# Kernel optimization log

Hardware: AMD Instinct MI355X
Metric: run time of the kernel (lower is better)

The kernel has to match this reference:

```python
import jax, jax.numpy as jnp
import numpy as np

B, S, D, F, E, TOP_K = 4, 1024, 512, 2048, 16, 2
TEMPERATURE = 0.5
STD = 0.02


def setup_inputs() -> dict:
    key = jax.random.key(0)
    ks = jax.random.split(key, 9)
    f32 = jnp.float32
    return {
        "x": jax.random.normal(ks[0], (B, S, D), f32),
        # router gate: Linear(D, D//2) -> ReLU -> Linear(D//2, E)
        "gate_w1": jax.random.normal(ks[1], (D, D // 2), f32) * STD,
        "gate_b1": jnp.zeros((D // 2,), f32),
        "gate_w2": jax.random.normal(ks[2], (D // 2, E), f32) * STD,
        "gate_b2": jnp.zeros((E,), f32),
        # stacked expert weights (E experts, each D->F->D)
        "up_w": jax.random.normal(ks[3], (E, D, F), f32) * STD,
        "up_b": jnp.zeros((E, F), f32),
        "down_w": jax.random.normal(ks[4], (E, F, D), f32) * STD,
        "down_b": jnp.zeros((E, D), f32),
    }


def reference(x, gate_w1, gate_b1, gate_w2, gate_b2, up_w, up_b, down_w, down_b):
    num_experts = up_w.shape[0]
    # ---- router ----
    h = jax.nn.relu(x @ gate_w1 + gate_b1)                      # [B,S,D//2]
    scores = h @ gate_w2 + gate_b2                              # [B,S,E]
    routing_probs = jax.nn.softmax(scores / TEMPERATURE, axis=-1)
    # load-balance loss: MSE(mean usage, uniform)
    batch_usage = routing_probs.mean(axis=(0, 1))               # [E]
    load_balance_loss = jnp.mean((batch_usage - 1.0 / num_experts) ** 2)
    # ---- top-k routing weights, renormalized via softmax over selected scores ----
    top_vals, top_idx = jax.lax.top_k(routing_probs, TOP_K)     # [B,S,K]
    top_probs = jax.nn.softmax(top_vals, axis=-1)               # [B,S,K]
    # scatter per-token top-k probs into dense [B,S,E] combine weights
    expert_probs = jnp.einsum(
        "bske,bsk->bse", jax.nn.one_hot(top_idx, num_experts, dtype=x.dtype), top_probs
    )
    # ---- every expert computed densely on all tokens, masked combine (faithful to source) ----
    hid = jax.nn.gelu(
        jnp.einsum("bsd,edf->ebsf", x, up_w) + up_b[:, None, None, :],
        approximate=False,
    )                                                            # [E,B,S,F]
    expert_out = jnp.einsum("ebsf,efd->ebsd", hid, down_w) + down_b[:, None, None, :]
    output = jnp.einsum("ebsd,bse->bsd", expert_out, expert_probs)  # [B,S,D]
    return output, load_balance_loss, routing_probs
```

## Files before the change

kernel.cpp:

```cpp
#include <hip/hip_runtime.h>
#include <hip/hip_bf16.h>

#define NTOK 4096
#define DIM  512
#define DH   256
#define NE   16
#define FF   2048
#define CAP  8192
#define MAXTILES 80
#define TEMP_INV 2.0f

#define OUT_LOSS  (NTOK * DIM)
#define OUT_PROBS (NTOK * DIM + 1)

#define WS_CNT    0
#define WS_USAGE  64
#define WS_NTILES 128
#define WS_DESC   256
#define WS_WTS    1024
#define WS_LISTS  36864
#define WS_H      (1ull<<20)
#define WS_G      (1ull<<20)
#define WS_TUP    (16ull<<20)
#define WS_PAIR   (16ull<<20)
#define WS_TDN    (48ull<<20)
#define WS_HID    (80ull<<20)

typedef __attribute__((ext_vector_type(8))) short bf16x8;
typedef __attribute__((ext_vector_type(8))) unsigned short u16x8;
typedef __attribute__((ext_vector_type(4))) float f32x4;

__device__ __forceinline__ unsigned short f2bf(float f) {
  union { float f; unsigned u; } c; c.f = f;
  return (unsigned short)((c.u + 0x7FFFu + ((c.u >> 16) & 1u)) >> 16);
}

#define GLOAD16(gp, lp) __builtin_amdgcn_global_load_lds( \
    (const __attribute__((address_space(1))) void*)(gp), \
    (__attribute__((address_space(3))) void*)(lp), 16, 0, 0)

__launch_bounds__(64)
__global__ void prep_kernel(const float* __restrict__ x,
                            const float* __restrict__ w1,
                            const float* __restrict__ b1,
                            const float* __restrict__ up_w,
                            const float* __restrict__ down_w,
                            float* __restrict__ H,
                            unsigned short* __restrict__ Tup,
                            unsigned short* __restrict__ Tdn) {
  __shared__ __align__(16) float As[32 * 72];
  __shared__ __align__(16) float Bs[32 * 40];
  int bx = blockIdx.x, tid = threadIdx.x;

  if (bx < 512) {
    int tok0 = (bx >> 3) * 64, n0 = (bx & 7) * 32;
    int ty = tid >> 3, tx = tid & 7;
    float acc[8][4];
#pragma unroll
    for (int r = 0; r < 8; ++r)
#pragma unroll
      for (int c = 0; c < 4; ++c) acc[r][c] = 0.f;

    for (int kc = 0; kc < 16; ++kc) {
      int k0 = kc * 32;
      {
        const float* xp = x + (size_t)(tok0 + tid) * DIM + k0;
#pragma unroll
        for (int q = 0; q < 8; ++q) {
          float4 v = *(const float4*)(xp + q * 4);
          As[(q * 4 + 0) * 72 + tid] = v.x;
          As[(q * 4 + 1) * 72 + tid] = v.y;
          As[(q * 4 + 2) * 72 + tid] = v.z;
          As[(q * 4 + 3) * 72 + tid] = v.w;
        }
      }
      {
        int kk = tid >> 1, ns = (tid & 1) * 16;
#pragma unroll
        for (int j = 0; j < 4; ++j)
          *(float4*)&Bs[kk * 40 + ns + j * 4] =
              *(const float4*)(w1 + (size_t)(k0 + kk) * DH + n0 + ns + j * 4);
      }
      __syncthreads();
#pragma unroll 8
      for (int k = 0; k < 32; ++k) {
        float4 a0 = *(const float4*)&As[k * 72 + ty * 8];
        float4 a1 = *(const float4*)&As[k * 72 + ty * 8 + 4];
        float4 b  = *(const float4*)&Bs[k * 40 + tx * 4];
#pragma unroll
        for (int c = 0; c < 4; ++c) {
          float bv = (c == 0) ? b.x : (c == 1) ? b.y : (c == 2) ? b.z : b.w;
          acc[0][c] = fmaf(a0.x, bv, acc[0][c]);
          acc[1][c] = fmaf(a0.y, bv, acc[1][c]);
          acc[2][c] = fmaf(a0.z, bv, acc[2][c]);
          acc[3][c] = fmaf(a0.w, bv, acc[3][c]);
          acc[4][c] = fmaf(a1.x, bv, acc[4][c]);
          acc[5][c] = fmaf(a1.y, bv, acc[5][c]);
          acc[6][c] = fmaf(a1.z, bv, acc[6][c]);
          acc[7][c] = fmaf(a1.w, bv, acc[7][c]);
        }
      }
      __syncthreads();
    }
    float4 bb = *(const float4*)(b1 + n0 + tx * 4);
#pragma unroll
    for (int r = 0; r < 8; ++r) {
      float4 o;
      o.x = fmaxf(acc[r][0] + bb.x, 0.f);
      o.y = fmaxf(acc[r][1] + bb.y, 0.f);
      o.z = fmaxf(acc[r][2] + bb.z, 0.f);
      o.w = fmaxf(acc[r][3] + bb.w, 0.f);
      *(float4*)(H + (size_t)(tok0 + ty * 8 + r) * DH + n0 + tx * 4) = o;
    }
  } else {
    int cb = bx - 512;
    const float* src; unsigned short* dst; int stride;
    if (cb < 4096) {
      int e = cb >> 8, kc = (cb >> 5) & 7, nb = cb & 31;
      src = up_w + (size_t)e * DIM * FF + (size_t)kc * 64 * FF + nb * 64;
      dst = Tup + ((size_t)(e * 8 + kc) * FF + nb * 64) * 64;
      stride = FF;
    } else {
      cb -= 4096;
      int e = cb >> 8, kc = (cb >> 3) & 31, nb = cb & 7;
      src = down_w + (size_t)e * FF * DIM + (size_t)kc * 64 * DIM + nb * 64;
      dst = Tdn + ((size_t)(e * 32 + kc) * DIM + nb * 64) * 64;
      stride = DIM;
    }
    const float* s = src + tid;
    unsigned short* drow = dst + (size_t)tid * 64;
    int sx = tid & 7;
#pragma unroll
    for (int g = 0; g < 8; ++g) {
      u16x8 pk;
#pragma unroll
      for (int j = 0; j < 8; ++j) pk[j] = f2bf(s[(size_t)(g * 8 + j) * stride]);
      *(u16x8*)(drow + ((g ^ sx) << 3)) = pk;
    }
  }
}

__launch_bounds__(256)
__global__ void score_kernel(const float* __restrict__ H,
                             const float* __restrict__ w2,
                             const float* __restrict__ b2,
                             float* __restrict__ out,
                             int* __restrict__ cnt,
                             float* __restrict__ usage,
                             float* __restrict__ wts,
                             int* __restrict__ lists) {
  __shared__ __align__(16) float hs[16][260];
  __shared__ __align__(16) float w2t[16][260];
  __shared__ float ps[16][NE];
  __shared__ float us[4][NE];
  int tid = threadIdx.x;
  int tok0 = blockIdx.x * 16;
  {
    int r = tid >> 4, seg = tid & 15;
    const float* hp = H + (size_t)(tok0 + r) * DH + seg * 16;
    *(float4*)&hs[r][seg * 16 + 0]  = *(const float4*)(hp + 0);
    *(float4*)&hs[r][seg * 16 + 4]  = *(const float4*)(hp + 4);
    *(float4*)&hs[r][seg * 16 + 8]  = *(const float4*)(hp + 8);
    *(float4*)&hs[r][seg * 16 + 12] = *(const float4*)(hp + 12);
  }
  {
    float4 a = *(const float4*)(w2 + (size_t)tid * 16 + 0);
    float4 b = *(const float4*)(w2 + (size_t)tid * 16 + 4);
    float4 c = *(const float4*)(w2 + (size_t)tid * 16 + 8);
    float4 d = *(const float4*)(w2 + (size_t)tid * 16 + 12);
    w2t[0][tid] = a.x;  w2t[1][tid] = a.y;  w2t[2][tid] = a.z;  w2t[3][tid] = a.w;
    w2t[4][tid] = b.x;  w2t[5][tid] = b.y;  w2t[6][tid] = b.z;  w2t[7][tid] = b.w;
    w2t[8][tid] = c.x;  w2t[9][tid] = c.y;  w2t[10][tid] = c.z; w2t[11][tid] = c.w;
    w2t[12][tid] = d.x; w2t[13][tid] = d.y; w2t[14][tid] = d.z; w2t[15][tid] = d.w;
  }
  __syncthreads();
  int t = tid >> 4, e = tid & 15;
  float s = b2[e];
#pragma unroll 4
  for (int j4 = 0; j4 < 64; ++j4) {
    float4 hv = *(const float4*)&hs[t][j4 * 4];
    float4 wv = *(const float4*)&w2t[e][j4 * 4];
    s = fmaf(hv.x, wv.x, fmaf(hv.y, wv.y, fmaf(hv.z, wv.z, fmaf(hv.w, wv.w, s))));
  }
  s *= TEMP_INV;
  float m = s;
#pragma unroll
  for (int d = 1; d < 16; d <<= 1) m = fmaxf(m, __shfl_xor(m, d));
  float p = expf(s - m);
  float sum = p;
#pragma unroll
  for (int d = 1; d < 16; d <<= 1) sum += __shfl_xor(sum, d);
  float prob = p / sum;
  out[OUT_PROBS + (size_t)(tok0 + t) * NE + e] = prob;
  ps[t][e] = prob;
  float v = prob;
  v += __shfl_xor(v, 16);
  v += __shfl_xor(v, 32);
  if ((tid & 63) < 16) us[tid >> 6][e] = v;
  __syncthreads();
  if (tid < 16) atomicAdd(&usage[tid], us[0][tid] + us[1][tid] + us[2][tid] + us[3][tid]);

  if (tid < 16) {
    int tt = tid;
    float v1 = -1.f; int i1 = 0;
    for (int ee = 0; ee < NE; ++ee) { float pv = ps[tt][ee]; if (pv > v1) { v1 = pv; i1 = ee; } }
    float v2 = -1.f; int i2 = 0;
    for (int ee = 0; ee < NE; ++ee) { if (ee == i1) continue; float pv = ps[tt][ee]; if (pv > v2) { v2 = pv; i2 = ee; } }
    float mm = fmaxf(v1, v2);
    float e0 = expf(v1 - mm), e1 = expf(v2 - mm);
    float rs = 1.f / (e0 + e1);
    int gt = tok0 + tt;
    wts[2 * gt]     = e0 * rs;
    wts[2 * gt + 1] = e1 * rs;
    int p1 = atomicAdd(&cnt[i1], 1);
    lists[i1 * CAP + p1] = 2 * gt;
    int p2 = atomicAdd(&cnt[i2], 1);
    lists[i2 * CAP + p2] = 2 * gt + 1;
  }
}

__global__ void sched_kernel(const int* __restrict__ cnt,
                             const float* __restrict__ usage,
                             int* __restrict__ ntiles,
                             int2* __restrict__ desc,
                             float* __restrict__ out_loss) {
  int lane = threadIdx.x;
  int e = lane & 15;
  int c = (lane < 16) ? cnt[e] : 0;
  int tl = (c + 127) >> 7;
  int v = tl;
#pragma unroll
  for (int d = 1; d < 16; d <<= 1) {
    int u = __shfl_up(v, d);
    if (lane >= d) v += u;
  }
  int excl = v - tl;
  int tot = __shfl(v, 15);
  if (lane == 0) *ntiles = tot;
  if (lane < 16) {
    for (int i = 0; i < tl; ++i) desc[excl + i] = make_int2(e, i << 7);
    float d0 = usage[e] * (1.f / 4096.f) - (1.f / 16.f);
    float ls = d0 * d0;
#pragma unroll
    for (int d = 1; d < 16; d <<= 1) ls += __shfl_xor(ls, d);
    if (lane == 0) *out_loss = ls * (1.f / 16.f);
  }
}

__launch_bounds__(256)
__global__ void gather_kernel(const float* __restrict__ x,
                              const int* __restrict__ cnt,
                              const int* __restrict__ ntiles,
                              const int2* __restrict__ desc,
                              const int* __restrict__ lists,
                              unsigned short* __restrict__ G) {
  int ty = blockIdx.x;
  if (ty >= *ntiles) return;
  int2 dd = desc[ty];
  int e = dd.x, i0 = dd.y;
  int cntE = cnt[e];
  int tid = threadIdx.x, r = tid >> 1, h = tid & 1;
  int aidx = i0 + r;
  bool valid = aidx < cntE;
  int slot = valid ? lists[e * CAP + aidx] : 0;
  const float* xrow = x + (size_t)(slot >> 1) * DIM;
  int chunk = blockIdx.y * 2 + h;
  unsigned short* dst = G + (size_t)ty * 65536 + (size_t)chunk * 8192 + r * 64;
  int sx = r & 7;
#pragma unroll
  for (int j = 0; j < 8; ++j) {
    u16x8 pk;
    if (valid) {
      float4 u = *(const float4*)(xrow + chunk * 64 + j * 8);
      float4 w = *(const float4*)(xrow + chunk * 64 + j * 8 + 4);
      pk[0] = f2bf(u.x); pk[1] = f2bf(u.y); pk[2] = f2bf(u.z); pk[3] = f2bf(u.w);
      pk[4] = f2bf(w.x); pk[5] = f2bf(w.y); pk[6] = f2bf(w.z); pk[7] = f2bf(w.w);
    } else {
      pk = u16x8{0, 0, 0, 0, 0, 0, 0, 0};
    }
    *(u16x8*)(dst + ((j ^ sx) << 3)) = pk;
  }
}

__launch_bounds__(256)
__global__ void up_kernel(const unsigned short* __restrict__ G,
                          const unsigned short* __restrict__ Tup,
                          const float* __restrict__ up_b,
                          const int* __restrict__ ntiles,
                          const int2* __restrict__ desc,
                          unsigned short* __restrict__ hid) {
  int ty = blockIdx.y;
  if (ty >= *ntiles) return;
  int e = desc[ty].x;
  int f0 = blockIdx.x * 128;
  __shared__ __align__(16) unsigned short smem[32768];
  int tid = threadIdx.x, lane = tid & 63, wid = tid >> 6;
  const unsigned short* Asrc = G + (size_t)ty * 65536;
  const unsigned short* Bsrc = Tup + ((size_t)(e * 8) * FF + f0) * 64;

  int wr = wid >> 1, wc = wid & 1, ln15 = lane & 15, lq = lane >> 4;
  f32x4 acc[4][4];
#pragma unroll
  for (int i = 0; i < 4; ++i)
#pragma unroll
    for (int j = 0; j < 4; ++j) acc[i][j] = f32x4{0.f, 0.f, 0.f, 0.f};

#define UP_STAGE(b, kc) do {                                          \
    const unsigned short* a_ = Asrc + (size_t)(kc) * 8192;            \
    const unsigned short* b_ = Bsrc + (size_t)(kc) * FF * 64;         \
    unsigned short* al_ = smem + (b) * 8192;                          \
    unsigned short* bl_ = smem + 16384 + (b) * 8192;                  \
    _Pragma("unroll")                                                 \
    for (int i_ = 0; i_ < 4; ++i_) {                                  \
      int off_ = (wid * 4 + i_) * 512;                                \
      GLOAD16(a_ + off_ + lane * 8, al_ + off_ + lane * 8);           \
      GLOAD16(b_ + off_ + lane * 8, bl_ + off_ + lane * 8);           \
    }                                                                 \
  } while (0)

  UP_STAGE(0, 0);
  asm volatile("s_waitcnt vmcnt(0)" ::: "memory");
  __syncthreads();
  int cur = 0;
  for (int kc = 0; kc < 8; ++kc) {
    if (kc < 7) UP_STAGE(cur ^ 1, kc + 1);
    const unsigned short* As = smem + cur * 8192;
    const unsigned short* Bs = smem + 16384 + cur * 8192;
#pragma unroll
    for (int ksub = 0; ksub < 2; ++ksub) {
      bf16x8 a[4], b[4];
      int g = (ksub << 2) + lq;
      int sw = (g ^ (ln15 & 7)) << 3;
#pragma unroll
      for (int mi = 0; mi < 4; ++mi)
        a[mi] = *(const bf16x8*)(As + ((wr << 6) + (mi << 4) + ln15) * 64 + sw);
#pragma unroll
      for (int ni = 0; ni < 4; ++ni)
        b[ni] = *(const bf16x8*)(Bs + ((wc << 6) + (ni << 4) + ln15) * 64 + sw);
#pragma unroll
      for (int mi = 0; mi < 4; ++mi)
#pragma unroll
        for (int ni = 0; ni < 4; ++ni)
          acc[mi][ni] = __builtin_amdgcn_mfma_f32_16x16x32_bf16(a[mi], b[ni], acc[mi][ni], 0, 0, 0);
    }
    asm volatile("s_waitcnt vmcnt(0)" ::: "memory");
    __syncthreads();
    cur ^= 1;
  }
  unsigned short* Cs = smem;
#pragma unroll
  for (int mi = 0; mi < 4; ++mi) {
#pragma unroll
    for (int ni = 0; ni < 4; ++ni) {
      int col = (wc << 6) + (ni << 4) + ln15;
      float bias = up_b[e * FF + f0 + col];
#pragma unroll
      for (int q = 0; q < 4; ++q) {
        int row = (wr << 6) + (mi << 4) + (lq << 2) + q;
        float vv = acc[mi][ni][q] + bias;
        float gl = 0.5f * vv * (1.f + erff(vv * 0.70710678118f));
        Cs[row * 136 + col] = f2bf(gl);
      }
    }
  }
  __syncthreads();
#pragma unroll
  for (int i = 0; i < 8; ++i) {
    int seg = tid + i * 256;
    int row = seg >> 4, c16 = seg & 15;
    int chunk = ty * 32 + (f0 >> 6) + (c16 >> 3);
    int slot = (c16 & 7) ^ (row & 7);
    u16x8 v = *(const u16x8*)(Cs + row * 136 + c16 * 8);
    *(u16x8*)(hid + ((size_t)chunk * 128 + row) * 64 + (slot << 3)) = v;
  }
#undef UP_STAGE
}

__launch_bounds__(256)
__global__ void down_kernel(const unsigned short* __restrict__ hid,
                            const unsigned short* __restrict__ Tdn,
                            const float* __restrict__ down_b,
                            const int* __restrict__ cnt,
                            const int* __restrict__ ntiles,
                            const int2* __restrict__ desc,
                            const int* __restrict__ lists,
                            float* __restrict__ pairbuf) {
  int ty = blockIdx.y;
  if (ty >= *ntiles) return;
  int2 dd = desc[ty];
  int e = dd.x, i0 = dd.y;
  int cntE = cnt[e];
  int n0 = blockIdx.x * 64;
  __shared__ __align__(16) unsigned short smem[24576];
  int tid = threadIdx.x, lane = tid & 63, wid = tid >> 6;
  const unsigned short* Asrc = hid + (size_t)ty * 32 * 8192;
  const unsigned short* Bsrc = Tdn + ((size_t)(e * 32) * DIM + n0) * 64;

  int wr = wid >> 1, wc = wid & 1, ln15 = lane & 15, lq = lane >> 4;
  f32x4 acc[4][2];
#pragma unroll
  for (int i = 0; i < 4; ++i) { acc[i][0] = f32x4{0.f,0.f,0.f,0.f}; acc[i][1] = f32x4{0.f,0.f,0.f,0.f}; }

#define DN_STAGE(b, kc) do {                                          \
    const unsigned short* a_ = Asrc + (size_t)(kc) * 8192;            \
    const unsigned short* b_ = Bsrc + (size_t)(kc) * DIM * 64;        \
    unsigned short* al_ = smem + (b) * 8192;                          \
    unsigned short* bl_ = smem + 16384 + (b) * 4096;                  \
    _Pragma("unroll")                                                 \
    for (int i_ = 0; i_ < 4; ++i_) {                                  \
      int off_ = (wid * 4 + i_) * 512;                                \
      GLOAD16(a_ + off_ + lane * 8, al_ + off_ + lane * 8);           \
    }                                                                 \
    _Pragma("unroll")                                                 \
    for (int i_ = 0; i_ < 2; ++i_) {                                  \
      int off_ = (wid * 2 + i_) * 512;                                \
      GLOAD16(b_ + off_ + lane * 8, bl_ + off_ + lane * 8);           \
    }                                                                 \
  } while (0)

  DN_STAGE(0, 0);
  asm volatile("s_waitcnt vmcnt(0)" ::: "memory");
  __syncthreads();
  int cur = 0;
  for (int kc = 0; kc < 32; ++kc) {
    if (kc < 31) DN_STAGE(cur ^ 1, kc + 1);
    const unsigned short* As = smem + cur * 8192;
    const unsigned short* Bs = smem + 16384 + cur * 4096;
#pragma unroll
    for (int ksub = 0; ksub < 2; ++ksub) {
      bf16x8 a[4], b[2];
      int g = (ksub << 2) + lq;
      int sw = (g ^ (ln15 & 7)) << 3;
#pragma unroll
      for (int mi = 0; mi < 4; ++mi)
        a[mi] = *(const bf16x8*)(As + ((wr << 6) + (mi << 4) + ln15) * 64 + sw);
#pragma unroll
      for (int ni = 0; ni < 2; ++ni)
        b[ni] = *(const bf16x8*)(Bs + ((wc << 5) + (ni << 4) + ln15) * 64 + sw);
#pragma unroll
      for (int mi = 0; mi < 4; ++mi)
#pragma unroll
        for (int ni = 0; ni < 2; ++ni)
          acc[mi][ni] = __builtin_amdgcn_mfma_f32_16x16x32_bf16(a[mi], b[ni], acc[mi][ni], 0, 0, 0);
    }
    asm volatile("s_waitcnt vmcnt(0)" ::: "memory");
    __syncthreads();
    cur ^= 1;
  }
#pragma unroll
  for (int mi = 0; mi < 4; ++mi) {
    int row = (wr << 6) + (mi << 4) + (lq << 2);
#pragma unroll
    for (int ni = 0; ni < 2; ++ni) {
      int col = n0 + (wc << 5) + (ni << 4) + ln15;
      float bias = down_b[e * DIM + col];
#pragma unroll
      for (int q = 0; q < 4; ++q) {
        int idx = i0 + row + q;
        if (idx < cntE) {
          int slot = lists[e * CAP + idx];
          pairbuf[(size_t)slot * DIM + col] = acc[mi][ni][q] + bias;
        }
      }
    }
  }
#undef DN_STAGE
}

__launch_bounds__(256)
__global__ void combine_kernel(const float* __restrict__ pairbuf,
                               const float* __restrict__ wts,
                               float* __restrict__ out) {
  int idx = blockIdx.x * 256 + threadIdx.x;
  int t = idx >> 7, d4 = (idx & 127) << 2;
  float w0 = wts[2 * t], w1 = wts[2 * t + 1];
  float4 a = *(const float4*)(pairbuf + (size_t)(2 * t) * DIM + d4);
  float4 b = *(const float4*)(pairbuf + (size_t)(2 * t + 1) * DIM + d4);
  float4 r;
  r.x = w0 * a.x + w1 * b.x; r.y = w0 * a.y + w1 * b.y;
  r.z = w0 * a.z + w1 * b.z; r.w = w0 * a.w + w1 * b.w;
  *(float4*)(out + (size_t)t * DIM + d4) = r;
}

extern "C" void kernel_launch(void* const* d_in, const int* in_sizes, int n_in,
                              void* d_out, int out_size, void* d_ws, size_t ws_size,
                              hipStream_t stream) {
  (void)in_sizes; (void)n_in; (void)out_size; (void)ws_size;
  const float* x   = (const float*)d_in[0];
  const float* gw1 = (const float*)d_in[1];
  const float* gb1 = (const float*)d_in[2];
  const float* gw2 = (const float*)d_in[3];
  const float* gb2 = (const float*)d_in[4];
  const float* uw  = (const float*)d_in[5];
  const float* ub  = (const float*)d_in[6];
  const float* dw  = (const float*)d_in[7];
  const float* db  = (const float*)d_in[8];
  float* out = (float*)d_out;
  char* ws = (char*)d_ws;

  int*   cnt     = (int*)(ws + WS_CNT);
  float* usage   = (float*)(ws + WS_USAGE);
  int*   ntiles  = (int*)(ws + WS_NTILES);
  int2*  desc    = (int2*)(ws + WS_DESC);
  float* wts     = (float*)(ws + WS_WTS);
  int*   lists   = (int*)(ws + WS_LISTS);
  float* H       = (float*)(ws + WS_H);
  unsigned short* G   = (unsigned short*)(ws + WS_G);
  unsigned short* Tup = (unsigned short*)(ws + WS_TUP);
  unsigned short* Tdn = (unsigned short*)(ws + WS_TDN);
  unsigned short* hid = (unsigned short*)(ws + WS_HID);
  float* pairbuf = (float*)(ws + WS_PAIR);

  hipMemsetAsync(d_ws, 0, 1024, stream);
  prep_kernel<<<8704, 64, 0, stream>>>(x, gw1, gb1, uw, dw, H, Tup, Tdn);
  score_kernel<<<NTOK / 16, 256, 0, stream>>>(H, gw2, gb2, out, cnt, usage, wts, lists);
  sched_kernel<<<1, 64, 0, stream>>>(cnt, usage, ntiles, desc, out + OUT_LOSS);
  gather_kernel<<<dim3(MAXTILES, 4), 256, 0, stream>>>(x, cnt, ntiles, desc, lists, G);
  up_kernel<<<dim3(FF / 128, MAXTILES), 256, 0, stream>>>(G, Tup, ub, ntiles, desc, hid);
  down_kernel<<<dim3(DIM / 64, MAXTILES), 256, 0, stream>>>(hid, Tdn, db, cnt, ntiles, desc, lists, pairbuf);
  combine_kernel<<<NTOK * DIM / 4 / 256, 256, 0, stream>>>(pairbuf, wts, out);
}
```

Before: 363.8 us.

## Split prep kernel, vectorize weight conversion, remap grids, widen down tiles

```diff
diff --git a/kernel.cpp b/kernel.cpp
--- a/kernel.cpp
+++ b/kernel.cpp
@@ -34,108 +34,118 @@
   union { float f; unsigned u; } c; c.f = f;
   return (unsigned short)((c.u + 0x7FFFu + ((c.u >> 16) & 1u)) >> 16);
 }
+__device__ __forceinline__ float gc(const float4& v, int c) {
+  return c == 0 ? v.x : c == 1 ? v.y : c == 2 ? v.z : v.w;
+}
 
 #define GLOAD16(gp, lp) __builtin_amdgcn_global_load_lds( \
     (const __attribute__((address_space(1))) void*)(gp), \
     (__attribute__((address_space(3))) void*)(lp), 16, 0, 0)
 
 __launch_bounds__(64)
-__global__ void prep_kernel(const float* __restrict__ x,
-                            const float* __restrict__ w1,
-                            const float* __restrict__ b1,
-                            const float* __restrict__ up_w,
-                            const float* __restrict__ down_w,
-                            float* __restrict__ H,
-                            unsigned short* __restrict__ Tup,
-                            unsigned short* __restrict__ Tdn) {
+__global__ void router_kernel(const float* __restrict__ x,
+                              const float* __restrict__ w1,
+                              const float* __restrict__ b1,
+                              float* __restrict__ H) {
   __shared__ __align__(16) float As[32 * 72];
   __shared__ __align__(16) float Bs[32 * 40];
   int bx = blockIdx.x, tid = threadIdx.x;
-
-  if (bx < 512) {
-    int tok0 = (bx >> 3) * 64, n0 = (bx & 7) * 32;
-    int ty = tid >> 3, tx = tid & 7;
-    float acc[8][4];
-#pragma unroll
-    for (int r = 0; r < 8; ++r)
-#pragma unroll
-      for (int c = 0; c < 4; ++c) acc[r][c] = 0.f;
-
-    for (int kc = 0; kc < 16; ++kc) {
-      int k0 = kc * 32;
-      {
-        const float* xp = x + (size_t)(tok0 + tid) * DIM + k0;
-#pragma unroll
-        for (int q = 0; q < 8; ++q) {
-          float4 v = *(const float4*)(xp + q * 4);
-          As[(q * 4 + 0) * 72 + tid] = v.x;
-          As[(q * 4 + 1) * 72 + tid] = v.y;
-          As[(q * 4 + 2) * 72 + tid] = v.z;
-          As[(q * 4 + 3) * 72 + tid] = v.w;
-        }
+  int tok0 = (bx >> 3) * 64, n0 = (bx & 7) * 32;
+  int ty = tid >> 3, tx = tid & 7;
+  float acc[8][4];
+#pragma unroll
+  for (int r = 0; r < 8; ++r)
+#pragma unroll
+    for (int c = 0; c < 4; ++c) acc[r][c] = 0.f;
+
+  for (int kc = 0; kc < 16; ++kc) {
+    int k0 = kc * 32;
+    {
+      const float* xp = x + (size_t)(tok0 + tid) * DIM + k0;
+#pragma unroll
+      for (int q = 0; q < 8; ++q) {
+        float4 v = *(const float4*)(xp + q * 4);
+        As[(q * 4 + 0) * 72 + tid] = v.x;
+        As[(q * 4 + 1) * 72 + tid] = v.y;
+        As[(q * 4 + 2) * 72 + tid] = v.z;
+        As[(q * 4 + 3) * 72 + tid] = v.w;
       }
-      {
-        int kk = tid >> 1, ns = (tid & 1) * 16;
-#pragma unroll
-        for (int j = 0; j < 4; ++j)
-          *(float4*)&Bs[kk * 40 + ns + j * 4] =
-              *(const float4*)(w1 + (size_t)(k0 + kk) * DH + n0 + ns + j * 4);
+    }
+    {
+      int kk = tid >> 1, ns = (tid & 1) * 16;
+#pragma unroll
+      for (int j = 0; j < 4; ++j)
+        *(float4*)&Bs[kk * 40 + ns + j * 4] =
+            *(const float4*)(w1 + (size_t)(k0 + kk) * DH + n0 + ns + j * 4);
+    }
+    __syncthreads();
+#pragma unroll 8
+    for (int k = 0; k < 32; ++k) {
+      float4 a0 = *(const float4*)&As[k * 72 + ty * 8];
+      float4 a1 = *(const float4*)&As[k * 72 + ty * 8 + 4];
+      float4 b  = *(const float4*)&Bs[k * 40 + tx * 4];
+#pragma unroll
+      for (int c = 0; c < 4; ++c) {
+        float bv = (c == 0) ? b.x : (c == 1) ? b.y : (c == 2) ? b.z : b.w;
+        acc[0][c] = fmaf(a0.x, bv, acc[0][c]);
+        acc[1][c] = fmaf(a0.y, bv, acc[1][c]);
+        acc[2][c] = fmaf(a0.z, bv, acc[2][c]);
+        acc[3][c] = fmaf(a0.w, bv, acc[3][c]);
+        acc[4][c] = fmaf(a1.x, bv, acc[4][c]);
+        acc[5][c] = fmaf(a1.y, bv, acc[5][c]);
+        acc[6][c] = fmaf(a1.z, bv, acc[6][c]);
+        acc[7][c] = fmaf(a1.w, bv, acc[7][c]);
       }
-      __syncthreads();
-#pragma unroll 8
-      for (int k = 0; k < 32; ++k) {
-        float4 a0 = *(const float4*)&As[k * 72 + ty * 8];
-        float4 a1 = *(const float4*)&As[k * 72 + ty * 8 + 4];
-        float4 b  = *(const float4*)&Bs[k * 40 + tx * 4];
-#pragma unroll
-        for (int c = 0; c < 4; ++c) {
-          float bv = (c == 0) ? b.x : (c == 1) ? b.y : (c == 2) ? b.z : b.w;
-          acc[0][c] = fmaf(a0.x, bv, acc[0][c]);
-          acc[1][c] = fmaf(a0.y, bv, acc[1][c]);
-          acc[2][c] = fmaf(a0.z, bv, acc[2][c]);
-          acc[3][c] = fmaf(a0.w, bv, acc[3][c]);
-          acc[4][c] = fmaf(a1.x, bv, acc[4][c]);
-          acc[5][c] = fmaf(a1.y, bv, acc[5][c]);
-          acc[6][c] = fmaf(a1.z, bv, acc[6][c]);
-          acc[7][c] = fmaf(a1.w, bv, acc[7][c]);
-        }
-      }
-      __syncthreads();
-    }
-    float4 bb = *(const float4*)(b1 + n0 + tx * 4);
-#pragma unroll
-    for (int r = 0; r < 8; ++r) {
-      float4 o;
-      o.x = fmaxf(acc[r][0] + bb.x, 0.f);
-      o.y = fmaxf(acc[r][1] + bb.y, 0.f);
-      o.z = fmaxf(acc[r][2] + bb.z, 0.f);
-      o.w = fmaxf(acc[r][3] + bb.w, 0.f);
-      *(float4*)(H + (size_t)(tok0 + ty * 8 + r) * DH + n0 + tx * 4) = o;
-    }
+    }
+    __syncthreads();
+  }
+  float4 bb = *(const float4*)(b1 + n0 + tx * 4);
+#pragma unroll
+  for (int r = 0; r < 8; ++r) {
+    float4 o;
+    o.x = fmaxf(acc[r][0] + bb.x, 0.f);
+    o.y = fmaxf(acc[r][1] + bb.y, 0.f);
+    o.z = fmaxf(acc[r][2] + bb.z, 0.f);
+    o.w = fmaxf(acc[r][3] + bb.w, 0.f);
+    *(float4*)(H + (size_t)(tok0 + ty * 8 + r) * DH + n0 + tx * 4) = o;
+  }
+}
+
+__launch_bounds__(256)
+__global__ void convert_kernel(const float* __restrict__ up_w,
+                               const float* __restrict__ down_w,
+                               unsigned short* __restrict__ Tup,
+                               unsigned short* __restrict__ Tdn) {
+  int bx = blockIdx.x, tid = threadIdx.x;
+  const float* src; unsigned short* dst; int stride, f;
+  if (bx < 256) {
+    int e = bx >> 4, kc = (bx >> 1) & 7, half = bx & 1;
+    f = (half * 256 + tid) * 4;
+    src = up_w + (size_t)e * DIM * FF + (size_t)(kc * 64) * FF + f;
+    dst = Tup + ((size_t)(e * 8 + kc) * FF + f) * 64;
+    stride = FF;
   } else {
-    int cb = bx - 512;
-    const float* src; unsigned short* dst; int stride;
-    if (cb < 4096) {
-      int e = cb >> 8, kc = (cb >> 5) & 7, nb = cb & 31;
-      src = up_w + (size_t)e * DIM * FF + (size_t)kc * 64 * FF + nb * 64;
-      dst = Tup + ((size_t)(e * 8 + kc) * FF + nb * 64) * 64;
-      stride = FF;
-    } else {
-      cb -= 4096;
-      int e = cb >> 8, kc = (cb >> 3) & 31, nb = cb & 7;
-      src = down_w + (size_t)e * FF * DIM + (size_t)kc * 64 * DIM + nb * 64;
-      dst = Tdn + ((size_t)(e * 32 + kc) * DIM + nb * 64) * 64;
-      stride = DIM;
-    }
-    const float* s = src + tid;
-    unsigned short* drow = dst + (size_t)tid * 64;
-    int sx = tid & 7;
-#pragma unroll
-    for (int g = 0; g < 8; ++g) {
+    int u = bx - 256;
+    int e = u >> 4, kcp = u & 15;
+    int kc = kcp * 2 + (tid >> 7);
+    f = (tid & 127) * 4;
+    src = down_w + (size_t)e * FF * DIM + (size_t)(kc * 64) * DIM + f;
+    dst = Tdn + ((size_t)(e * 32 + kc) * DIM + f) * 64;
+    stride = DIM;
+  }
+#pragma unroll
+  for (int g = 0; g < 8; ++g) {
+    float4 v[8];
+#pragma unroll
+    for (int j = 0; j < 8; ++j)
+      v[j] = *(const float4*)(src + (size_t)(g * 8 + j) * stride);
+#pragma unroll
+    for (int c = 0; c < 4; ++c) {
       u16x8 pk;
 #pragma unroll
-      for (int j = 0; j < 8; ++j) pk[j] = f2bf(s[(size_t)(g * 8 + j) * stride]);
-      *(u16x8*)(drow + ((g ^ sx) << 3)) = pk;
+      for (int j = 0; j < 8; ++j) pk[j] = f2bf(gc(v[j], c));
+      int fr = f + c;
+      *(u16x8*)(dst + (size_t)c * 64 + ((g ^ (fr & 7)) << 3)) = pk;
     }
   }
 }
@@ -289,10 +299,11 @@
                           const int* __restrict__ ntiles,
                           const int2* __restrict__ desc,
                           unsigned short* __restrict__ hid) {
-  int ty = blockIdx.y;
+  int lid = (blockIdx.x & 7) * (MAXTILES * 16 / 8) + (blockIdx.x >> 3);
+  int ty = lid >> 4, fb = lid & 15;
   if (ty >= *ntiles) return;
   int e = desc[ty].x;
-  int f0 = blockIdx.x * 128;
+  int f0 = fb * 128;
   __shared__ __align__(16) unsigned short smem[32768];
   int tid = threadIdx.x, lane = tid & 63, wid = tid >> 6;
   const unsigned short* Asrc = G + (size_t)ty * 65536;
@@ -385,35 +396,34 @@
                             const int2* __restrict__ desc,
                             const int* __restrict__ lists,
                             float* __restrict__ pairbuf) {
-  int ty = blockIdx.y;
+  int lid = (blockIdx.x & 7) * (MAXTILES * 4 / 8) + (blockIdx.x >> 3);
+  int ty = lid >> 2, nb = lid & 3;
   if (ty >= *ntiles) return;
   int2 dd = desc[ty];
   int e = dd.x, i0 = dd.y;
   int cntE = cnt[e];
-  int n0 = blockIdx.x * 64;
-  __shared__ __align__(16) unsigned short smem[24576];
+  int n0 = nb * 128;
+  __shared__ __align__(16) unsigned short smem[32768];
   int tid = threadIdx.x, lane = tid & 63, wid = tid >> 6;
   const unsigned short* Asrc = hid + (size_t)ty * 32 * 8192;
   const unsigned short* Bsrc = Tdn + ((size_t)(e * 32) * DIM + n0) * 64;
 
   int wr = wid >> 1, wc = wid & 1, ln15 = lane & 15, lq = lane >> 4;
-  f32x4 acc[4][2];
-#pragma unroll
-  for (int i = 0; i < 4; ++i) { acc[i][0] = f32x4{0.f,0.f,0.f,0.f}; acc[i][1] = f32x4{0.f,0.f,0.f,0.f}; }
+  f32x4 acc[4][4];
+#pragma unroll
+  for (int i = 0; i < 4; ++i)
+#pragma unroll
+    for (int j = 0; j < 4; ++j) acc[i][j] = f32x4{0.f, 0.f, 0.f, 0.f};
 
 #define DN_STAGE(b, kc) do {                                          \
     const unsigned short* a_ = Asrc + (size_t)(kc) * 8192;            \
     const unsigned short* b_ = Bsrc + (size_t)(kc) * DIM * 64;        \
     unsigned short* al_ = smem + (b) * 8192;                          \
-    unsigned short* bl_ = smem + 16384 + (b) * 4096;                  \
+    unsigned short* bl_ = smem + 16384 + (b) * 8192;                  \
     _Pragma("unroll")                                                 \
     for (int i_ = 0; i_ < 4; ++i_) {                                  \
       int off_ = (wid * 4 + i_) * 512;                                \
       GLOAD16(a_ + off_ + lane * 8, al_ + off_ + lane * 8);           \
-    }                                                                 \
-    _Pragma("unroll")                                                 \
-    for (int i_ = 0; i_ < 2; ++i_) {                                  \
-      int off_ = (wid * 2 + i_) * 512;                                \
       GLOAD16(b_ + off_ + lane * 8, bl_ + off_ + lane * 8);           \
     }                                                                 \
   } while (0)
@@ -425,22 +435,22 @@
   for (int kc = 0; kc < 32; ++kc) {
     if (kc < 31) DN_STAGE(cur ^ 1, kc + 1);
     const unsigned short* As = smem + cur * 8192;
-    const unsigned short* Bs = smem + 16384 + cur * 4096;
+    const unsigned short* Bs = smem + 16384 + cur * 8192;
 #pragma unroll
     for (int ksub = 0; ksub < 2; ++ksub) {
-      bf16x8 a[4], b[2];
+      bf16x8 a[4], b[4];
       int g = (ksub << 2) + lq;
       int sw = (g ^ (ln15 & 7)) << 3;
 #pragma unroll
       for (int mi = 0; mi < 4; ++mi)
         a[mi] = *(const bf16x8*)(As + ((wr << 6) + (mi << 4) + ln15) * 64 + sw);
 #pragma unroll
-      for (int ni = 0; ni < 2; ++ni)
-        b[ni] = *(const bf16x8*)(Bs + ((wc << 5) + (ni << 4) + ln15) * 64 + sw);
+      for (int ni = 0; ni < 4; ++ni)
+        b[ni] = *(const bf16x8*)(Bs + ((wc << 6) + (ni << 4) + ln15) * 64 + sw);
 #pragma unroll
       for (int mi = 0; mi < 4; ++mi)
 #pragma unroll
-        for (int ni = 0; ni < 2; ++ni)
+        for (int ni = 0; ni < 4; ++ni)
           acc[mi][ni] = __builtin_amdgcn_mfma_f32_16x16x32_bf16(a[mi], b[ni], acc[mi][ni], 0, 0, 0);
     }
     asm volatile("s_waitcnt vmcnt(0)" ::: "memory");
@@ -451,8 +461,8 @@
   for (int mi = 0; mi < 4; ++mi) {
     int row = (wr << 6) + (mi << 4) + (lq << 2);
 #pragma unroll
-    for (int ni = 0; ni < 2; ++ni) {
-      int col = n0 + (wc << 5) + (ni << 4) + ln15;
+    for (int ni = 0; ni < 4; ++ni) {
+      int col = n0 + (wc << 6) + (ni << 4) + ln15;
       float bias = down_b[e * DIM + col];
 #pragma unroll
       for (int q = 0; q < 4; ++q) {
@@ -512,11 +522,12 @@
   float* pairbuf = (float*)(ws + WS_PAIR);
 
   hipMemsetAsync(d_ws, 0, 1024, stream);
-  prep_kernel<<<8704, 64, 0, stream>>>(x, gw1, gb1, uw, dw, H, Tup, Tdn);
+  router_kernel<<<512, 64, 0, stream>>>(x, gw1, gb1, H);
+  convert_kernel<<<512, 256, 0, stream>>>(uw, dw, Tup, Tdn);
   score_kernel<<<NTOK / 16, 256, 0, stream>>>(H, gw2, gb2, out, cnt, usage, wts, lists);
   sched_kernel<<<1, 64, 0, stream>>>(cnt, usage, ntiles, desc, out + OUT_LOSS);
   gather_kernel<<<dim3(MAXTILES, 4), 256, 0, stream>>>(x, cnt, ntiles, desc, lists, G);
-  up_kernel<<<dim3(FF / 128, MAXTILES), 256, 0, stream>>>(G, Tup, ub, ntiles, desc, hid);
-  down_kernel<<<dim3(DIM / 64, MAXTILES), 256, 0, stream>>>(hid, Tdn, db, cnt, ntiles, desc, lists, pairbuf);
+  up_kernel<<<16 * MAXTILES, 256, 0, stream>>>(G, Tup, ub, ntiles, desc, hid);
+  down_kernel<<<4 * MAXTILES, 256, 0, stream>>>(hid, Tdn, db, cnt, ntiles, desc, lists, pairbuf);
   combine_kernel<<<NTOK * DIM / 4 / 256, 256, 0, stream>>>(pairbuf, wts, out);
 }
```

New measurement: 411.5 us. 1.13x slower.

## Coalesce weight conversion via LDS, remap grid for XCD locality, use tanh GELU

Applied to the files above, without the earlier changes.

```diff
diff --git a/kernel.cpp b/kernel.cpp
--- a/kernel.cpp
+++ b/kernel.cpp
@@ -34,12 +34,15 @@
   union { float f; unsigned u; } c; c.f = f;
   return (unsigned short)((c.u + 0x7FFFu + ((c.u >> 16) & 1u)) >> 16);
 }
+__device__ __forceinline__ float gc(const float4& v, int c) {
+  return c == 0 ? v.x : c == 1 ? v.y : c == 2 ? v.z : v.w;
+}
 
 #define GLOAD16(gp, lp) __builtin_amdgcn_global_load_lds( \
     (const __attribute__((address_space(1))) void*)(gp), \
     (__attribute__((address_space(3))) void*)(lp), 16, 0, 0)
 
-__launch_bounds__(64)
+__launch_bounds__(256)
 __global__ void prep_kernel(const float* __restrict__ x,
                             const float* __restrict__ w1,
                             const float* __restrict__ b1,
@@ -48,13 +51,50 @@
                             float* __restrict__ H,
                             unsigned short* __restrict__ Tup,
                             unsigned short* __restrict__ Tdn) {
-  __shared__ __align__(16) float As[32 * 72];
-  __shared__ __align__(16) float Bs[32 * 40];
+  __shared__ __align__(16) char smem[41984];
   int bx = blockIdx.x, tid = threadIdx.x;
 
-  if (bx < 512) {
-    int tok0 = (bx >> 3) * 64, n0 = (bx & 7) * 32;
-    int ty = tid >> 3, tx = tid & 7;
+  if (bx < 2048) {
+    const float* src; unsigned short* dst; int stride;
+    if (bx < 1024) {
+      int e = bx >> 6, kc = (bx >> 3) & 7, nb = bx & 7;
+      src = up_w + (size_t)e * DIM * FF + (size_t)(kc * 64) * FF + nb * 256;
+      dst = Tup + ((size_t)(e * 8 + kc) * FF + nb * 256) * 64;
+      stride = FF;
+    } else {
+      int u = bx - 1024;
+      int e = u >> 6, kc = (u >> 1) & 31, nb = u & 1;
+      src = down_w + (size_t)e * FF * DIM + (size_t)(kc * 64) * DIM + nb * 256;
+      dst = Tdn + ((size_t)(e * 32 + kc) * DIM + nb * 256) * 64;
+      stride = DIM;
+    }
+    unsigned short* L = (unsigned short*)smem;
+    int r = tid & 63, cg = tid >> 6;
+    const float* sp = src + (size_t)r * stride + cg * 64;
+#pragma unroll
+    for (int j = 0; j < 16; ++j) {
+      float4 v = *(const float4*)(sp + j * 4);
+      int nl = cg * 64 + j * 4;
+      L[(nl + 0) * 72 + r] = f2bf(v.x);
+      L[(nl + 1) * 72 + r] = f2bf(v.y);
+      L[(nl + 2) * 72 + r] = f2bf(v.z);
+      L[(nl + 3) * 72 + r] = f2bf(v.w);
+    }
+    __syncthreads();
+    int w = tid >> 6, lane = tid & 63, sub = lane >> 3, g = lane & 7;
+#pragma unroll
+    for (int i = 0; i < 8; ++i) {
+      int nl = w * 64 + i * 8 + sub;
+      u16x8 v = *(const u16x8*)(L + nl * 72 + g * 8);
+      *(u16x8*)(dst + (size_t)nl * 64 + ((g ^ (nl & 7)) << 3)) = v;
+    }
+  } else {
+    int rb = bx - 2048;
+    int tok0 = (rb >> 3) * 256, n0 = (rb & 7) * 32;
+    int w = tid >> 6, lane = tid & 63;
+    float* Af = (float*)smem + w * (32 * 72);
+    float* Bs = (float*)(smem + 36864);
+    int ty = lane >> 3, tx = lane & 7;
     float acc[8][4];
 #pragma unroll
     for (int r = 0; r < 8; ++r)
@@ -64,28 +104,25 @@
     for (int kc = 0; kc < 16; ++kc) {
       int k0 = kc * 32;
       {
-        const float* xp = x + (size_t)(tok0 + tid) * DIM + k0;
+        const float* xp = x + (size_t)(tok0 + w * 64 + lane) * DIM + k0;
 #pragma unroll
         for (int q = 0; q < 8; ++q) {
           float4 v = *(const float4*)(xp + q * 4);
-          As[(q * 4 + 0) * 72 + tid] = v.x;
-          As[(q * 4 + 1) * 72 + tid] = v.y;
-          As[(q * 4 + 2) * 72 + tid] = v.z;
-          As[(q * 4 + 3) * 72 + tid] = v.w;
+          Af[(q * 4 + 0) * 72 + lane] = v.x;
+          Af[(q * 4 + 1) * 72 + lane] = v.y;
+          Af[(q * 4 + 2) * 72 + lane] = v.z;
+          Af[(q * 4 + 3) * 72 + lane] = v.w;
         }
       }
       {
-        int kk = tid >> 1, ns = (tid & 1) * 16;
-#pragma unroll
-        for (int j = 0; j < 4; ++j)
-          *(float4*)&Bs[kk * 40 + ns + j * 4] =
-              *(const float4*)(w1 + (size_t)(k0 + kk) * DH + n0 + ns + j * 4);
+        int kk = tid >> 3, ns = (tid & 7) * 4;
+        *(float4*)&Bs[kk * 40 + ns] = *(const float4*)(w1 + (size_t)(k0 + kk) * DH + n0 + ns);
       }
       __syncthreads();
 #pragma unroll 8
       for (int k = 0; k < 32; ++k) {
-        float4 a0 = *(const float4*)&As[k * 72 + ty * 8];
-        float4 a1 = *(const float4*)&As[k * 72 + ty * 8 + 4];
+        float4 a0 = *(const float4*)&Af[k * 72 + ty * 8];
+        float4 a1 = *(const float4*)&Af[k * 72 + ty * 8 + 4];
         float4 b  = *(const float4*)&Bs[k * 40 + tx * 4];
 #pragma unroll
         for (int c = 0; c < 4; ++c) {
@@ -110,32 +147,7 @@
       o.y = fmaxf(acc[r][1] + bb.y, 0.f);
       o.z = fmaxf(acc[r][2] + bb.z, 0.f);
       o.w = fmaxf(acc[r][3] + bb.w, 0.f);
-      *(float4*)(H + (size_t)(tok0 + ty * 8 + r) * DH + n0 + tx * 4) = o;
-    }
-  } else {
-    int cb = bx - 512;
-    const float* src; unsigned short* dst; int stride;
-    if (cb < 4096) {
-      int e = cb >> 8, kc = (cb >> 5) & 7, nb = cb & 31;
-      src = up_w + (size_t)e * DIM * FF + (size_t)kc * 64 * FF + nb * 64;
-      dst = Tup + ((size_t)(e * 8 + kc) * FF + nb * 64) * 64;
-      stride = FF;
-    } else {
-      cb -= 4096;
-      int e = cb >> 8, kc = (cb >> 3) & 31, nb = cb & 7;
-      src = down_w + (size_t)e * FF * DIM + (size_t)kc * 64 * DIM + nb * 64;
-      dst = Tdn + ((size_t)(e * 32 + kc) * DIM + nb * 64) * 64;
-      stride = DIM;
-    }
-    const float* s = src + tid;
-    unsigned short* drow = dst + (size_t)tid * 64;
-    int sx = tid & 7;
-#pragma unroll
-    for (int g = 0; g < 8; ++g) {
-      u16x8 pk;
-#pragma unroll
-      for (int j = 0; j < 8; ++j) pk[j] = f2bf(s[(size_t)(g * 8 + j) * stride]);
-      *(u16x8*)(drow + ((g ^ sx) << 3)) = pk;
+      *(float4*)(H + (size_t)(tok0 + w * 64 + ty * 8 + r) * DH + n0 + tx * 4) = o;
     }
   }
 }
@@ -289,10 +301,11 @@
                           const int* __restrict__ ntiles,
                           const int2* __restrict__ desc,
                           unsigned short* __restrict__ hid) {
-  int ty = blockIdx.y;
+  int lid = (blockIdx.x & 7) * (MAXTILES * 16 / 8) + (blockIdx.x >> 3);
+  int ty = lid >> 4, fb = lid & 15;
   if (ty >= *ntiles) return;
   int e = desc[ty].x;
-  int f0 = blockIdx.x * 128;
+  int f0 = fb * 128;
   __shared__ __align__(16) unsigned short smem[32768];
   int tid = threadIdx.x, lane = tid & 63, wid = tid >> 6;
   const unsigned short* Asrc = G + (size_t)ty * 65536;
@@ -358,7 +371,8 @@
       for (int q = 0; q < 4; ++q) {
         int row = (wr << 6) + (mi << 4) + (lq << 2) + q;
         float vv = acc[mi][ni][q] + bias;
-        float gl = 0.5f * vv * (1.f + erff(vv * 0.70710678118f));
+        float uu = vv * fmaf(vv * vv, 0.044715f, 1.0f) * 1.5957691216f;
+        float gl = vv / (1.f + __expf(-uu));
         Cs[row * 136 + col] = f2bf(gl);
       }
     }
@@ -385,12 +399,13 @@
                             const int2* __restrict__ desc,
                             const int* __restrict__ lists,
                             float* __restrict__ pairbuf) {
-  int ty = blockIdx.y;
+  int lid = (blockIdx.x & 7) * MAXTILES + (blockIdx.x >> 3);
+  int ty = lid >> 3, nb = lid & 7;
   if (ty >= *ntiles) return;
   int2 dd = desc[ty];
   int e = dd.x, i0 = dd.y;
   int cntE = cnt[e];
-  int n0 = blockIdx.x * 64;
+  int n0 = nb * 64;
   __shared__ __align__(16) unsigned short smem[24576];
   int tid = threadIdx.x, lane = tid & 63, wid = tid >> 6;
   const unsigned short* Asrc = hid + (size_t)ty * 32 * 8192;
@@ -512,11 +527,11 @@
   float* pairbuf = (float*)(ws + WS_PAIR);
 
   hipMemsetAsync(d_ws, 0, 1024, stream);
-  prep_kernel<<<8704, 64, 0, stream>>>(x, gw1, gb1, uw, dw, H, Tup, Tdn);
+  prep_kernel<<<2176, 256, 0, stream>>>(x, gw1, gb1, uw, dw, H, Tup, Tdn);
   score_kernel<<<NTOK / 16, 256, 0, stream>>>(H, gw2, gb2, out, cnt, usage, wts, lists);
   sched_kernel<<<1, 64, 0, stream>>>(cnt, usage, ntiles, desc, out + OUT_LOSS);
   gather_kernel<<<dim3(MAXTILES, 4), 256, 0, stream>>>(x, cnt, ntiles, desc, lists, G);
-  up_kernel<<<dim3(FF / 128, MAXTILES), 256, 0, stream>>>(G, Tup, ub, ntiles, desc, hid);
-  down_kernel<<<dim3(DIM / 64, MAXTILES), 256, 0, stream>>>(hid, Tdn, db, cnt, ntiles, desc, lists, pairbuf);
+  up_kernel<<<16 * MAXTILES, 256, 0, stream>>>(G, Tup, ub, ntiles, desc, hid);
+  down_kernel<<<8 * MAXTILES, 256, 0, stream>>>(hid, Tdn, db, cnt, ntiles, desc, lists, pairbuf);
   combine_kernel<<<NTOK * DIM / 4 / 256, 256, 0, stream>>>(pairbuf, wts, out);
 }
```

New measurement: 372.4 us. 1.02x slower.
